# Performance work log

Measured on AMD Instinct MI355X. Metric: run time of the kernel, lower is better.

## Reference

```python
import jax, jax.numpy as jnp
import numpy as np

EMBED_DIM = 1024
FFN_DIM = 4096
N_QUBITS = 16
BATCH, SEQ = 4, 2048


def setup_inputs() -> dict:
    key = jax.random.key(0)
    ks = jax.random.split(key, 6)
    s1 = 1.0 / np.sqrt(EMBED_DIM)
    s2 = 1.0 / np.sqrt(FFN_DIM)
    s3 = 1.0 / np.sqrt(N_QUBITS)
    return {
        "x": jax.random.normal(ks[0], (BATCH, SEQ, EMBED_DIM), jnp.float32),
        "W1": jax.random.normal(ks[1], (FFN_DIM, EMBED_DIM), jnp.float32) * s1,
        "Wq": jax.random.normal(ks[2], (N_QUBITS, FFN_DIM), jnp.float32) * s2,
        "theta": jax.random.normal(ks[3], (N_QUBITS,), jnp.float32),
        "W2": jax.random.normal(ks[4], (FFN_DIM, N_QUBITS), jnp.float32) * s3,
        "Wo": jax.random.normal(ks[5], (EMBED_DIM, FFN_DIM), jnp.float32) * s2,
    }


def reference(x, W1, Wq, theta, W2, Wo):
    # linear1: [b,s,e] @ [f,e]^T -> [b,s,f]
    h = jnp.einsum('bse,fe->bsf', x, W1)
    # to_qubits: [b,s,f] -> [b,s,q]
    q = jnp.einsum('bsf,qf->bsq', h, Wq)
    # Quantum circuit: RX(q_i) encoding then trainable RX(theta_i) per wire,
    # wires are unentangled product states -> <Z_i> = cos(q_i + theta_i).
    qm = jnp.cos(q + theta)
    # linear2 + relu
    h2 = jax.nn.relu(jnp.einsum('bsq,fq->bsf', qm, W2))
    # out_proj (dropout is identity in eval / p=0)
    return jnp.einsum('bsf,ef->bse', h2, Wo)
```

## Files before the change

### kernel.cpp

```cpp
#include <hip/hip_runtime.h>
#include <hip/hip_bf16.h>
#include <math.h>

typedef _Float16 f16;
typedef __attribute__((ext_vector_type(8))) _Float16 f16x8;
typedef __attribute__((ext_vector_type(4))) _Float16 f16x4;
typedef __attribute__((ext_vector_type(4))) float f32x4;

#define M_TOT 8192
#define E_DIM 1024
#define F_DIM 4096
#define NQ    16

#define BARRIER() asm volatile("s_barrier" ::: "memory")
#define WAITV(n)  asm volatile("s_waitcnt vmcnt(" #n ")" ::: "memory")
#define WAITLGKM() asm volatile("s_waitcnt lgkmcnt(0)" ::: "memory")

__device__ __forceinline__ f16x8 cvt8(float4 a, float4 b) {
    f16x8 o;
    o[0] = (f16)a.x; o[1] = (f16)a.y; o[2] = (f16)a.z; o[3] = (f16)a.w;
    o[4] = (f16)b.x; o[5] = (f16)b.y; o[6] = (f16)b.z; o[7] = (f16)b.w;
    return o;
}

__global__ __launch_bounds__(256) void prep_kernel(
    const float* __restrict__ W1, f16* __restrict__ W1t,
    const float* __restrict__ wo, f16* __restrict__ woh,
    const float* __restrict__ W2, f16* __restrict__ w2p)
{
    __shared__ float ls[64][68];
    const int b = blockIdx.x;
    if (b < 1024) {
        const int bf = b & 63;
        const int be = b >> 6;
        const int t  = threadIdx.x;
        const int r  = t >> 4;
        const int c4 = (t & 15) * 4;
        #pragma unroll
        for (int i = 0; i < 4; ++i) {
            int fr = r + i * 16;
            float4 v = *reinterpret_cast<const float4*>(W1 + (size_t)(bf * 64 + fr) * E_DIM + be * 64 + c4);
            ls[fr][c4] = v.x; ls[fr][c4 + 1] = v.y; ls[fr][c4 + 2] = v.z; ls[fr][c4 + 3] = v.w;
        }
        __syncthreads();
        const int er = t >> 2;
        const int fc = (t & 3) * 16;
        f16x8 o0, o1;
        #pragma unroll
        for (int j = 0; j < 8; ++j) { o0[j] = (f16)ls[fc + j][er]; o1[j] = (f16)ls[fc + 8 + j][er]; }
        f16* dst = W1t + (size_t)(be * 64 + er) * F_DIM + bf * 64 + fc;
        *reinterpret_cast<f16x8*>(dst)     = o0;
        *reinterpret_cast<f16x8*>(dst + 8) = o1;
    } else if (b < 3072) {
        size_t i = ((size_t)(b - 1024) * 256 + threadIdx.x) * 8;
        float4 v0 = *reinterpret_cast<const float4*>(wo + i);
        float4 v1 = *reinterpret_cast<const float4*>(wo + i + 4);
        *reinterpret_cast<f16x8*>(woh + i) = cvt8(v0, v1);
    } else {
        int t = (b - 3072) * 256 + threadIdx.x;
        size_t i = (size_t)t * 8;
        int col = (int)(i & 31);
        f16x8 o;
        if (col < NQ) {
            int row = (int)(i >> 5);
            float4 v0 = *reinterpret_cast<const float4*>(W2 + (size_t)row * NQ + col);
            float4 v1 = *reinterpret_cast<const float4*>(W2 + (size_t)row * NQ + col + 4);
            o = cvt8(v0, v1);
        } else {
            for (int k = 0; k < 8; ++k) o[k] = (f16)0.f;
        }
        *reinterpret_cast<f16x8*>(w2p + i) = o;
    }
}

__global__ __launch_bounds__(256) void tg_kernel(
    const float* __restrict__ Wq, const f16* __restrict__ W1t,
    float* __restrict__ pT)
{
    const int w = threadIdx.x >> 6, lane = threadIdx.x & 63;
    const int fr = lane & 15, fq = lane >> 4;
    const int kc = blockIdx.x & 15;
    const int et = blockIdx.x >> 4;
    const int e0 = et * 128 + w * 32;
    const int kbase = kc * 256;

    f32x4 acc[2] = {};
    #pragma unroll
    for (int s = 0; s < 8; ++s) {
        int k = kbase + s * 32 + fq * 8;
        float4 a0 = *reinterpret_cast<const float4*>(Wq + (size_t)fr * F_DIM + k);
        float4 a1 = *reinterpret_cast<const float4*>(Wq + (size_t)fr * F_DIM + k + 4);
        f16x8 af = cvt8(a0, a1);
        #pragma unroll
        for (int n = 0; n < 2; ++n) {
            f16x8 bf = *reinterpret_cast<const f16x8*>(W1t + (size_t)(e0 + n * 16 + fr) * F_DIM + k);
            acc[n] = __builtin_amdgcn_mfma_f32_16x16x32_f16(af, bf, acc[n], 0, 0, 0);
        }
    }
    #pragma unroll
    for (int n = 0; n < 2; ++n)
        #pragma unroll
        for (int j = 0; j < 4; ++j)
            pT[(size_t)kc * (16 * E_DIM) + (size_t)(fq * 4 + j) * E_DIM + e0 + n * 16 + fr] = acc[n][j];
}

__global__ __launch_bounds__(256) void treduce_kernel(
    const float* __restrict__ pT, f16* __restrict__ Th)
{
    int idx = blockIdx.x * 256 + threadIdx.x;
    float s = 0.f;
    #pragma unroll
    for (int kc = 0; kc < 16; ++kc) s += pT[(size_t)kc * (16 * E_DIM) + idx];
    Th[idx] = (f16)s;
}

__global__ __launch_bounds__(512) void qx2_kernel(
    const float* __restrict__ x, const f16* __restrict__ Th,
    const float* __restrict__ theta, f16* __restrict__ qmp)
{
    __shared__ __align__(16) f16 ths[16 * 1024];
    __shared__ float pql[2048];
    const int tid = threadIdx.x, w = tid >> 6, lane = tid & 63;
    const int fr = lane & 15, fq = lane >> 4;
    const int m0 = blockIdx.x * 64;

    #pragma unroll
    for (int i = 0; i < 4; ++i) {
        int tau = i * 512 + tid;
        int q   = tau >> 7;
        int kb  = tau & 127;
        f16x8 v = *reinterpret_cast<const f16x8*>(Th + (size_t)q * E_DIM + kb * 8);
        int boff = (q * 2048 + kb * 16) ^ ((q & 7) << 4);
        *reinterpret_cast<f16x8*>((char*)ths + boff) = v;
    }
    __syncthreads();

    const int kc = w >> 2;
    const int rg = w & 3;
    const float* xa = x + (size_t)(m0 + rg * 16 + fr) * E_DIM + kc * 512;
    f32x4 acc = {};
    #pragma unroll
    for (int s = 0; s < 16; ++s) {
        int ko = s * 32 + fq * 8;
        float4 a0 = *reinterpret_cast<const float4*>(xa + ko);
        float4 a1 = *reinterpret_cast<const float4*>(xa + ko + 4);
        f16x8 af = cvt8(a0, a1);
        int boff = (fr * 2048 + (kc * 512 + ko) * 2) ^ ((fr & 7) << 4);
        f16x8 bf = *reinterpret_cast<const f16x8*>((char*)ths + boff);
        acc = __builtin_amdgcn_mfma_f32_16x16x32_f16(af, bf, acc, 0, 0, 0);
    }
    #pragma unroll
    for (int j = 0; j < 4; ++j)
        pql[(kc * 64 + rg * 16 + fq * 4 + j) * 16 + fr] = acc[j];
    __syncthreads();

    #pragma unroll
    for (int e = 0; e < 2; ++e) {
        int idx = e * 512 + tid;
        int row = idx >> 4, q = idx & 15;
        float s = pql[idx] + pql[1024 + idx];
        float v = cosf(s + theta[q]);
        qmp[(size_t)(m0 + row) * 32 + q]      = (f16)v;
        qmp[(size_t)(m0 + row) * 32 + 16 + q] = (f16)0.f;
    }
}

__device__ __forceinline__ void gload_lds16(const f16* g, f16* l) {
    __builtin_amdgcn_global_load_lds(
        (const __attribute__((address_space(1))) void*)(g),
        (__attribute__((address_space(3))) void*)(l), 16, 0, 0);
}

__global__ __launch_bounds__(512, 2)
void gemm4f(const f16* __restrict__ qmp, const f16* __restrict__ w2p,
            const f16* __restrict__ Wo, f16* __restrict__ P0, f16* __restrict__ P1)
{
    extern __shared__ __align__(16) f16 smem[];
    const int tid  = threadIdx.x;
    const int w    = tid >> 6;
    const int lane = tid & 63;

    const int nwg = gridDim.x;
    const int bid = blockIdx.x;
    const int cpx = nwg >> 3;
    int swz = (bid & 7) * cpx + (bid >> 3);
    const int per = nwg >> 1;
    const int split = swz / per;
    const int r = swz % per;
    const int by = r >> 2, bx = r & 3;
    const int m0 = by * 256, n0 = bx * 256;

    const int wr = w >> 2, wc = w & 3;
    const int fr = lane & 15, fq = lane >> 4;
    const int K = 2048;

    const f16* Bb  = Wo + (size_t)split * K;
    const f16* w2g = w2p + (size_t)split * K * 32;
    f16* Pout = split ? P1 : P0;

    const int r0w = w * 32 + fr;
    f16x8 qreg0 = *reinterpret_cast<const f16x8*>(qmp + (size_t)(m0 + r0w) * 32 + fq * 8);
    f16x8 qreg1 = *reinterpret_cast<const f16x8*>(qmp + (size_t)(m0 + r0w + 16) * 32 + fq * 8);

    const int rl   = w * 8 + (lane >> 3);
    const int scol = (((lane & 7) ^ (rl & 7)) * 8);
    const f16* gB = Bb + (size_t)(n0 + rl) * F_DIM + scol;
    f16* lB = smem + 16384 + w * 512;

#define SB(b,h,j,kt) gload_lds16(gB + (size_t)((h)*128 + (j)*64) * F_DIM + (kt), lB + (b)*32768 + (h)*8192 + (j)*4096)
#define SBH(b,h,kt) do { SB(b,h,0,kt); SB(b,h,1,kt); } while(0)

    f16x8 w2a[4], w2b[4];
#define LOADW2(R, kt) do { _Pragma("unroll") \
    for (int ft = 0; ft < 4; ++ft) \
        R[ft] = *reinterpret_cast<const f16x8*>(w2g + (size_t)((kt) + ft*16 + fr) * 32 + fq * 8); } while(0)

#define PWRITE(bdst, ft, C0, C1) do {                                             \
    f16x4 h0_, h1_;                                                               \
    _Pragma("unroll") for (int jj = 0; jj < 4; ++jj) {                            \
        h0_[jj] = (f16)fmaxf(C0[jj], 0.f); h1_[jj] = (f16)fmaxf(C1[jj], 0.f); }   \
    const int sl_ = (2 * (ft) + (fq >> 1)) ^ (fr & 7);                            \
    *reinterpret_cast<f16x4*>(smem + (bdst)*32768 + (r0w)*64    + sl_*8 + ((fq & 1) << 2)) = h0_; \
    *reinterpret_cast<f16x4*>(smem + (bdst)*32768 + (r0w+16)*64 + sl_*8 + ((fq & 1) << 2)) = h1_; \
    } while(0)

#define PRODUCE(bdst, W2R) do {                                                   \
    f32x4 z_ = {0.f, 0.f, 0.f, 0.f};                                              \
    _Pragma("unroll") for (int ft = 0; ft < 4; ++ft) {                            \
        f32x4 c0_ = __builtin_amdgcn_mfma_f32_16x16x32_f16(W2R[ft], qreg0, z_, 0, 0, 0); \
        f32x4 c1_ = __builtin_amdgcn_mfma_f32_16x16x32_f16(W2R[ft], qreg1, z_, 0, 0, 0); \
        PWRITE(bdst, ft, c0_, c1_);                                               \
    } } while(0)

    const int xm  = fr & 7;
    const int so0 = ((0 + fq) ^ xm) * 8;
    const int so1 = ((4 + fq) ^ xm) * 8;
    const int aro = (wr * 128 + fr) * 64;
    const int bro = (wc * 64  + fr) * 64;

#define AF(b,m,ks) (*reinterpret_cast<const f16x8*>(smem + (b)*32768 + aro + (m)*1024 + so##ks))
#define BF(b,n,ks) (*reinterpret_cast<const f16x8*>(smem + (b)*32768 + 16384 + bro + (n)*1024 + so##ks))

    f32x4 acc[8][4] = {};
    f16x8 bf[4][2];

#define MAINMMA(p, a00, a01, a10, a11)                                            \
    _Pragma("unroll") for (int n = 0; n < 4; ++n) {                               \
        acc[2*(p)  ][n] = __builtin_amdgcn_mfma_f32_16x16x32_f16(a00, bf[n][0], acc[2*(p)  ][n], 0,0,0); \
        acc[2*(p)+1][n] = __builtin_amdgcn_mfma_f32_16x16x32_f16(a10, bf[n][0], acc[2*(p)+1][n], 0,0,0); } \
    _Pragma("unroll") for (int n = 0; n < 4; ++n) {                               \
        acc[2*(p)  ][n] = __builtin_amdgcn_mfma_f32_16x16x32_f16(a01, bf[n][1], acc[2*(p)  ][n], 0,0,0); \
        acc[2*(p)+1][n] = __builtin_amdgcn_mfma_f32_16x16x32_f16(a11, bf[n][1], acc[2*(p)+1][n], 0,0,0); }

#define PHASE(b, p, STAGES, W4) do {                                              \
    f16x8 a00 = AF(b, 2*(p),   0), a01 = AF(b, 2*(p),   1);                       \
    f16x8 a10 = AF(b, 2*(p)+1, 0), a11 = AF(b, 2*(p)+1, 1);                       \
    if ((p) == 0) { _Pragma("unroll")                                             \
        for (int n = 0; n < 4; ++n) { bf[n][0] = BF(b,n,0); bf[n][1] = BF(b,n,1); } } \
    STAGES;                                                                       \
    BARRIER();                                                                    \
    __builtin_amdgcn_s_setprio(1);                                                \
    MAINMMA(p, a00, a01, a10, a11);                                               \
    __builtin_amdgcn_s_setprio(0);                                                \
    if (W4) { WAITV(8); WAITLGKM(); }                                             \
    BARRIER(); } while(0)

#define PHASEP(b, bdst, W2R) do {                                                 \
    f16x8 a00 = AF(b, 0, 0), a01 = AF(b, 0, 1);                                   \
    f16x8 a10 = AF(b, 1, 0), a11 = AF(b, 1, 1);                                   \
    _Pragma("unroll")                                                             \
    for (int n = 0; n < 4; ++n) { bf[n][0] = BF(b,n,0); bf[n][1] = BF(b,n,1); }   \
    BARRIER();                                                                    \
    __builtin_amdgcn_s_setprio(1);                                                \
    f32x4 z_ = {0.f, 0.f, 0.f, 0.f};                                              \
    f32x4 c00 = __builtin_amdgcn_mfma_f32_16x16x32_f16(W2R[0], qreg0, z_, 0,0,0); \
    f32x4 c10 = __builtin_amdgcn_mfma_f32_16x16x32_f16(W2R[0], qreg1, z_, 0,0,0); \
    f32x4 c01 = __builtin_amdgcn_mfma_f32_16x16x32_f16(W2R[1], qreg0, z_, 0,0,0); \
    f32x4 c11 = __builtin_amdgcn_mfma_f32_16x16x32_f16(W2R[1], qreg1, z_, 0,0,0); \
    f32x4 c02 = __builtin_amdgcn_mfma_f32_16x16x32_f16(W2R[2], qreg0, z_, 0,0,0); \
    f32x4 c12 = __builtin_amdgcn_mfma_f32_16x16x32_f16(W2R[2], qreg1, z_, 0,0,0); \
    f32x4 c03 = __builtin_amdgcn_mfma_f32_16x16x32_f16(W2R[3], qreg0, z_, 0,0,0); \
    f32x4 c13 = __builtin_amdgcn_mfma_f32_16x16x32_f16(W2R[3], qreg1, z_, 0,0,0); \
    MAINMMA(0, a00, a01, a10, a11);                                               \
    __builtin_amdgcn_s_setprio(0);                                                \
    PWRITE(bdst, 0, c00, c10); PWRITE(bdst, 1, c01, c11);                         \
    PWRITE(bdst, 2, c02, c12); PWRITE(bdst, 3, c03, c13);                         \
    BARRIER(); } while(0)

    const int NT = K >> 6;
    const int NI = NT >> 1;

    LOADW2(w2b, 0);
    LOADW2(w2a, 64);
    SBH(0,0,0);  SBH(0,1,0);
    SBH(1,0,64); SBH(1,1,64);
    WAITV(0);
    BARRIER();
    PRODUCE(0, w2b);
    WAITLGKM();
    BARRIER();

    for (int i = 0; i < NI; ++i) {
        int t2 = 2*i+2; if (t2 > NT-1) t2 = NT-1;
        int t3 = 2*i+3; if (t3 > NT-1) t3 = NT-1;
        const int k2 = t2 << 6, k3 = t3 << 6;
        PHASEP(0, 1, w2a);
        PHASE(0, 1, LOADW2(w2b, k2); SBH(0,0,k2), 0);
        PHASE(0, 2, SBH(0,1,k2),                0);
        PHASE(0, 3, ,                           1);
        PHASEP(1, 0, w2b);
        PHASE(1, 1, LOADW2(w2a, k3); SBH(1,0,k3), 0);
        PHASE(1, 2, SBH(1,1,k3),                0);
        PHASE(1, 3, ,                           1);
    }
    WAITV(0);

    #pragma unroll
    for (int m = 0; m < 8; ++m) {
        #pragma unroll
        for (int n = 0; n < 4; ++n) {
            #pragma unroll
            for (int j = 0; j < 4; ++j) {
                int row = m0 + wr * 128 + m * 16 + fq * 4 + j;
                int col = n0 + wc * 64  + n * 16 + fr;
                Pout[(size_t)row * E_DIM + col] = (f16)acc[m][n][j];
            }
        }
    }
#undef SB
#undef SBH
#undef LOADW2
#undef PWRITE
#undef PRODUCE
#undef AF
#undef BF
#undef MAINMMA
#undef PHASE
#undef PHASEP
}

__global__ __launch_bounds__(256) void out_reduce2_kernel(
    float* __restrict__ out, const f16* __restrict__ p0, const f16* __restrict__ p1)
{
    size_t i = ((size_t)blockIdx.x * 256 + threadIdx.x) * 8;
    f16x8 a = *reinterpret_cast<const f16x8*>(p0 + i);
    f16x8 b = *reinterpret_cast<const f16x8*>(p1 + i);
    float4 v0, v1;
    v0.x = (float)a[0] + (float)b[0]; v0.y = (float)a[1] + (float)b[1];
    v0.z = (float)a[2] + (float)b[2]; v0.w = (float)a[3] + (float)b[3];
    v1.x = (float)a[4] + (float)b[4]; v1.y = (float)a[5] + (float)b[5];
    v1.z = (float)a[6] + (float)b[6]; v1.w = (float)a[7] + (float)b[7];
    *reinterpret_cast<float4*>(out + i)     = v0;
    *reinterpret_cast<float4*>(out + i + 4) = v1;
}

extern "C" void kernel_launch(void* const* d_in, const int* in_sizes, int n_in,
                              void* d_out, int out_size, void* d_ws, size_t ws_size,
                              hipStream_t stream) {
    const float* x  = (const float*)d_in[0];
    const float* W1 = (const float*)d_in[1];
    const float* Wq = (const float*)d_in[2];
    const float* th = (const float*)d_in[3];
    const float* W2 = (const float*)d_in[4];
    const float* Wo = (const float*)d_in[5];
    float* out = (float*)d_out;

    char* base = (char*)d_ws;
    float* pT  = (float*)base;
    f16*   Th  = (f16*)(base + (1 << 20));
    f16*   w1t = (f16*)(base + 16777216);
    f16*   woh = w1t + (size_t)E_DIM * F_DIM;
    f16*   w2p = woh + (size_t)E_DIM * F_DIM;
    f16*   qmp = w2p + (size_t)F_DIM * 32;
    f16*   p0  = qmp + (size_t)M_TOT * 32;
    f16*   p1  = p0  + (size_t)M_TOT * E_DIM;

    static bool attr_done = false;
    if (!attr_done) {
        hipFuncSetAttribute((const void*)&gemm4f,
                            hipFuncAttributeMaxDynamicSharedMemorySize, 131072);
        attr_done = true;
    }

    prep_kernel<<<3136, 256, 0, stream>>>(W1, w1t, Wo, woh, W2, w2p);
    tg_kernel<<<128, 256, 0, stream>>>(Wq, w1t, pT);
    treduce_kernel<<<64, 256, 0, stream>>>(pT, Th);
    qx2_kernel<<<128, 512, 0, stream>>>(x, Th, th, qmp);
    gemm4f<<<256, 512, 131072, stream>>>(qmp, w2p, woh, p0, p1);
    out_reduce2_kernel<<<4096, 256, 0, stream>>>(out, p0, p1);
}
```

Measured before the change: 116.9 us.

## Replace split-K 256x256 GEMM with full-K 128x128 tiles writing fp32 output directly

The final fused linear2+relu+out_proj GEMM drops its two-way split-K scheme, which wrote two fp16 partial buffers and needed a separate reduce kernel. It now uses 128x128 tiles with 256 threads over the full K of 4096, launches 512 blocks and writes fp32 results straight to the output. The produce step that regenerates h2 tiles is folded into phase 0 of the pipeline. This removes the partial-buffer round trip and one kernel launch, and drops the fp16 rounding of partial sums. In exchange, each tile has less reuse of the regenerated h2 and Wo data than the larger tile did.

Measured after the change: 118.5 us. About the same (+1.4%).

```diff
diff --git a/kernel.cpp b/kernel.cpp
--- a/kernel.cpp
+++ b/kernel.cpp
@@ -171,9 +171,9 @@
         (__attribute__((address_space(3))) void*)(l), 16, 0, 0);
 }
 
-__global__ __launch_bounds__(512, 2)
-void gemm4f(const f16* __restrict__ qmp, const f16* __restrict__ w2p,
-            const f16* __restrict__ Wo, f16* __restrict__ P0, f16* __restrict__ P1)
+__global__ __launch_bounds__(256, 2)
+void gemm4f(const f16* __restrict__ qmp, const f16* __restrict__ w2g,
+            const f16* __restrict__ woh, float* __restrict__ out)
 {
     extern __shared__ __align__(16) f16 smem[];
     const int tid  = threadIdx.x;
@@ -184,31 +184,23 @@
     const int bid = blockIdx.x;
     const int cpx = nwg >> 3;
     int swz = (bid & 7) * cpx + (bid >> 3);
-    const int per = nwg >> 1;
-    const int split = swz / per;
-    const int r = swz % per;
-    const int by = r >> 2, bx = r & 3;
-    const int m0 = by * 256, n0 = bx * 256;
-
-    const int wr = w >> 2, wc = w & 3;
+    const int by = swz & 63, bx = swz >> 6;
+    const int m0 = by * 128, n0 = bx * 128;
+
+    const int wr = w >> 1, wc = w & 1;
     const int fr = lane & 15, fq = lane >> 4;
-    const int K = 2048;
-
-    const f16* Bb  = Wo + (size_t)split * K;
-    const f16* w2g = w2p + (size_t)split * K * 32;
-    f16* Pout = split ? P1 : P0;
+    const int K = 4096;
 
     const int r0w = w * 32 + fr;
     f16x8 qreg0 = *reinterpret_cast<const f16x8*>(qmp + (size_t)(m0 + r0w) * 32 + fq * 8);
     f16x8 qreg1 = *reinterpret_cast<const f16x8*>(qmp + (size_t)(m0 + r0w + 16) * 32 + fq * 8);
 
-    const int rl   = w * 8 + (lane >> 3);
-    const int scol = (((lane & 7) ^ (rl & 7)) * 8);
-    const f16* gB = Bb + (size_t)(n0 + rl) * F_DIM + scol;
-    f16* lB = smem + 16384 + w * 512;
-
-#define SB(b,h,j,kt) gload_lds16(gB + (size_t)((h)*128 + (j)*64) * F_DIM + (kt), lB + (b)*32768 + (h)*8192 + (j)*4096)
-#define SBH(b,h,kt) do { SB(b,h,0,kt); SB(b,h,1,kt); } while(0)
+    const int rl   = tid >> 3;
+    const int scol = ((lane & 7) ^ (rl & 7)) * 8;
+    const f16* gB = woh + (size_t)(n0 + rl) * F_DIM + scol;
+    f16* lBw = smem + 8192 + w * 512;
+
+#define SB(b,j,kt) gload_lds16(gB + (size_t)((j)*32) * F_DIM + (kt), lBw + (b)*16384 + (j)*2048)
 
     f16x8 w2a[4], w2b[4];
 #define LOADW2(R, kt) do { _Pragma("unroll") \
@@ -220,8 +212,8 @@
     _Pragma("unroll") for (int jj = 0; jj < 4; ++jj) {                            \
         h0_[jj] = (f16)fmaxf(C0[jj], 0.f); h1_[jj] = (f16)fmaxf(C1[jj], 0.f); }   \
     const int sl_ = (2 * (ft) + (fq >> 1)) ^ (fr & 7);                            \
-    *reinterpret_cast<f16x4*>(smem + (bdst)*32768 + (r0w)*64    + sl_*8 + ((fq & 1) << 2)) = h0_; \
-    *reinterpret_cast<f16x4*>(smem + (bdst)*32768 + (r0w+16)*64 + sl_*8 + ((fq & 1) << 2)) = h1_; \
+    *reinterpret_cast<f16x4*>(smem + (bdst)*16384 + (r0w)*64    + sl_*8 + ((fq & 1) << 2)) = h0_; \
+    *reinterpret_cast<f16x4*>(smem + (bdst)*16384 + (r0w+16)*64 + sl_*8 + ((fq & 1) << 2)) = h1_; \
     } while(0)
 
 #define PRODUCE(bdst, W2R) do {                                                   \
@@ -235,65 +227,37 @@
     const int xm  = fr & 7;
     const int so0 = ((0 + fq) ^ xm) * 8;
     const int so1 = ((4 + fq) ^ xm) * 8;
-    const int aro = (wr * 128 + fr) * 64;
-    const int bro = (wc * 64  + fr) * 64;
-
-#define AF(b,m,ks) (*reinterpret_cast<const f16x8*>(smem + (b)*32768 + aro + (m)*1024 + so##ks))
-#define BF(b,n,ks) (*reinterpret_cast<const f16x8*>(smem + (b)*32768 + 16384 + bro + (n)*1024 + so##ks))
-
-    f32x4 acc[8][4] = {};
+    const int aro = (wr * 64 + fr) * 64;
+    const int bro = (wc * 64 + fr) * 64;
+
+#define AF(b,m,ks) (*reinterpret_cast<const f16x8*>(smem + (b)*16384 + aro + (m)*1024 + so##ks))
+#define BF(b,n,ks) (*reinterpret_cast<const f16x8*>(smem + (b)*16384 + 8192 + bro + (n)*1024 + so##ks))
+
+    f32x4 acc[4][4] = {};
     f16x8 bf[4][2];
 
-#define MAINMMA(p, a00, a01, a10, a11)                                            \
-    _Pragma("unroll") for (int n = 0; n < 4; ++n) {                               \
-        acc[2*(p)  ][n] = __builtin_amdgcn_mfma_f32_16x16x32_f16(a00, bf[n][0], acc[2*(p)  ][n], 0,0,0); \
-        acc[2*(p)+1][n] = __builtin_amdgcn_mfma_f32_16x16x32_f16(a10, bf[n][0], acc[2*(p)+1][n], 0,0,0); } \
-    _Pragma("unroll") for (int n = 0; n < 4; ++n) {                               \
-        acc[2*(p)  ][n] = __builtin_amdgcn_mfma_f32_16x16x32_f16(a01, bf[n][1], acc[2*(p)  ][n], 0,0,0); \
-        acc[2*(p)+1][n] = __builtin_amdgcn_mfma_f32_16x16x32_f16(a11, bf[n][1], acc[2*(p)+1][n], 0,0,0); }
-
 #define PHASE(b, p, STAGES, W4) do {                                              \
-    f16x8 a00 = AF(b, 2*(p),   0), a01 = AF(b, 2*(p),   1);                       \
-    f16x8 a10 = AF(b, 2*(p)+1, 0), a11 = AF(b, 2*(p)+1, 1);                       \
+    f16x8 a0 = AF(b, p, 0), a1 = AF(b, p, 1);                                     \
     if ((p) == 0) { _Pragma("unroll")                                             \
         for (int n = 0; n < 4; ++n) { bf[n][0] = BF(b,n,0); bf[n][1] = BF(b,n,1); } } \
     STAGES;                                                                       \
     BARRIER();                                                                    \
     __builtin_amdgcn_s_setprio(1);                                                \
-    MAINMMA(p, a00, a01, a10, a11);                                               \
+    _Pragma("unroll") for (int n = 0; n < 4; ++n)                                 \
+        acc[p][n] = __builtin_amdgcn_mfma_f32_16x16x32_f16(a0, bf[n][0], acc[p][n], 0,0,0); \
+    _Pragma("unroll") for (int n = 0; n < 4; ++n)                                 \
+        acc[p][n] = __builtin_amdgcn_mfma_f32_16x16x32_f16(a1, bf[n][1], acc[p][n], 0,0,0); \
     __builtin_amdgcn_s_setprio(0);                                                \
     if (W4) { WAITV(8); WAITLGKM(); }                                             \
     BARRIER(); } while(0)
 
-#define PHASEP(b, bdst, W2R) do {                                                 \
-    f16x8 a00 = AF(b, 0, 0), a01 = AF(b, 0, 1);                                   \
-    f16x8 a10 = AF(b, 1, 0), a11 = AF(b, 1, 1);                                   \
-    _Pragma("unroll")                                                             \
-    for (int n = 0; n < 4; ++n) { bf[n][0] = BF(b,n,0); bf[n][1] = BF(b,n,1); }   \
-    BARRIER();                                                                    \
-    __builtin_amdgcn_s_setprio(1);                                                \
-    f32x4 z_ = {0.f, 0.f, 0.f, 0.f};                                              \
-    f32x4 c00 = __builtin_amdgcn_mfma_f32_16x16x32_f16(W2R[0], qreg0, z_, 0,0,0); \
-    f32x4 c10 = __builtin_amdgcn_mfma_f32_16x16x32_f16(W2R[0], qreg1, z_, 0,0,0); \
-    f32x4 c01 = __builtin_amdgcn_mfma_f32_16x16x32_f16(W2R[1], qreg0, z_, 0,0,0); \
-    f32x4 c11 = __builtin_amdgcn_mfma_f32_16x16x32_f16(W2R[1], qreg1, z_, 0,0,0); \
-    f32x4 c02 = __builtin_amdgcn_mfma_f32_16x16x32_f16(W2R[2], qreg0, z_, 0,0,0); \
-    f32x4 c12 = __builtin_amdgcn_mfma_f32_16x16x32_f16(W2R[2], qreg1, z_, 0,0,0); \
-    f32x4 c03 = __builtin_amdgcn_mfma_f32_16x16x32_f16(W2R[3], qreg0, z_, 0,0,0); \
-    f32x4 c13 = __builtin_amdgcn_mfma_f32_16x16x32_f16(W2R[3], qreg1, z_, 0,0,0); \
-    MAINMMA(0, a00, a01, a10, a11);                                               \
-    __builtin_amdgcn_s_setprio(0);                                                \
-    PWRITE(bdst, 0, c00, c10); PWRITE(bdst, 1, c01, c11);                         \
-    PWRITE(bdst, 2, c02, c12); PWRITE(bdst, 3, c03, c13);                         \
-    BARRIER(); } while(0)
-
     const int NT = K >> 6;
     const int NI = NT >> 1;
 
     LOADW2(w2b, 0);
     LOADW2(w2a, 64);
-    SBH(0,0,0);  SBH(0,1,0);
-    SBH(1,0,64); SBH(1,1,64);
+    SB(0,0,0);  SB(0,1,0);  SB(0,2,0);  SB(0,3,0);
+    SB(1,0,64); SB(1,1,64); SB(1,2,64); SB(1,3,64);
     WAITV(0);
     BARRIER();
     PRODUCE(0, w2b);
@@ -304,54 +268,36 @@
         int t2 = 2*i+2; if (t2 > NT-1) t2 = NT-1;
         int t3 = 2*i+3; if (t3 > NT-1) t3 = NT-1;
         const int k2 = t2 << 6, k3 = t3 << 6;
-        PHASEP(0, 1, w2a);
-        PHASE(0, 1, LOADW2(w2b, k2); SBH(0,0,k2), 0);
-        PHASE(0, 2, SBH(0,1,k2),                0);
-        PHASE(0, 3, ,                           1);
-        PHASEP(1, 0, w2b);
-        PHASE(1, 1, LOADW2(w2a, k3); SBH(1,0,k3), 0);
-        PHASE(1, 2, SBH(1,1,k3),                0);
-        PHASE(1, 3, ,                           1);
+        PHASE(0, 0, PRODUCE(1, w2a),                     0);
+        PHASE(0, 1, LOADW2(w2b, k2); SB(0,0,k2); SB(0,1,k2), 0);
+        PHASE(0, 2, SB(0,2,k2); SB(0,3,k2),              0);
+        PHASE(0, 3, ,                                    1);
+        PHASE(1, 0, PRODUCE(0, w2b),                     0);
+        PHASE(1, 1, LOADW2(w2a, k3); SB(1,0,k3); SB(1,1,k3), 0);
+        PHASE(1, 2, SB(1,2,k3); SB(1,3,k3),              0);
+        PHASE(1, 3, ,                                    1);
     }
     WAITV(0);
 
     #pragma unroll
-    for (int m = 0; m < 8; ++m) {
+    for (int m = 0; m < 4; ++m) {
         #pragma unroll
         for (int n = 0; n < 4; ++n) {
             #pragma unroll
             for (int j = 0; j < 4; ++j) {
-                int row = m0 + wr * 128 + m * 16 + fq * 4 + j;
-                int col = n0 + wc * 64  + n * 16 + fr;
-                Pout[(size_t)row * E_DIM + col] = (f16)acc[m][n][j];
+                int row = m0 + wr * 64 + m * 16 + fq * 4 + j;
+                int col = n0 + wc * 64 + n * 16 + fr;
+                out[(size_t)row * E_DIM + col] = acc[m][n][j];
             }
         }
     }
 #undef SB
-#undef SBH
 #undef LOADW2
 #undef PWRITE
 #undef PRODUCE
 #undef AF
 #undef BF
-#undef MAINMMA
 #undef PHASE
-#undef PHASEP
-}
-
-__global__ __launch_bounds__(256) void out_reduce2_kernel(
-    float* __restrict__ out, const f16* __restrict__ p0, const f16* __restrict__ p1)
-{
-    size_t i = ((size_t)blockIdx.x * 256 + threadIdx.x) * 8;
-    f16x8 a = *reinterpret_cast<const f16x8*>(p0 + i);
-    f16x8 b = *reinterpret_cast<const f16x8*>(p1 + i);
-    float4 v0, v1;
-    v0.x = (float)a[0] + (float)b[0]; v0.y = (float)a[1] + (float)b[1];
-    v0.z = (float)a[2] + (float)b[2]; v0.w = (float)a[3] + (float)b[3];
-    v1.x = (float)a[4] + (float)b[4]; v1.y = (float)a[5] + (float)b[5];
-    v1.z = (float)a[6] + (float)b[6]; v1.w = (float)a[7] + (float)b[7];
-    *reinterpret_cast<float4*>(out + i)     = v0;
-    *reinterpret_cast<float4*>(out + i + 4) = v1;
 }
 
 extern "C" void kernel_launch(void* const* d_in, const int* in_sizes, int n_in,
@@ -372,13 +318,11 @@
     f16*   woh = w1t + (size_t)E_DIM * F_DIM;
     f16*   w2p = woh + (size_t)E_DIM * F_DIM;
     f16*   qmp = w2p + (size_t)F_DIM * 32;
-    f16*   p0  = qmp + (size_t)M_TOT * 32;
-    f16*   p1  = p0  + (size_t)M_TOT * E_DIM;
 
     static bool attr_done = false;
     if (!attr_done) {
         hipFuncSetAttribute((const void*)&gemm4f,
-                            hipFuncAttributeMaxDynamicSharedMemorySize, 131072);
+                            hipFuncAttributeMaxDynamicSharedMemorySize, 65536);
         attr_done = true;
     }
 
@@ -386,6 +330,5 @@
     tg_kernel<<<128, 256, 0, stream>>>(Wq, w1t, pT);
     treduce_kernel<<<64, 256, 0, stream>>>(pT, Th);
     qx2_kernel<<<128, 512, 0, stream>>>(x, Th, th, qmp);
-    gemm4f<<<256, 512, 131072, stream>>>(qmp, w2p, woh, p0, p1);
-    out_reduce2_kernel<<<4096, 256, 0, stream>>>(out, p0, p1);
-}
+    gemm4f<<<512, 256, 65536, stream>>>(qmp, w2p, woh, out);
+}
```
